# Optimization experiments

Measured on AMD Instinct MI355X. Metric: run time of the kernel, lower is better.

## Reference

```python
import jax, jax.numpy as jnp
import numpy as np
from jax import lax

NUM_ITER = 10
SMOOTH = 1.0


def _minpool(x, wh, ww):
    # stride-1 min pool with SAME padding (pad value +inf, ignored by min)
    return lax.reduce_window(x, np.inf, lax.min, (1, 1, wh, ww), (1, 1, 1, 1), 'SAME')


def _maxpool(x, wh, ww):
    return lax.reduce_window(x, -np.inf, lax.max, (1, 1, wh, ww), (1, 1, 1, 1), 'SAME')


def soft_erode(img):
    # min of separable 3x1 and 1x3 min-pools (== -maxpool(-img) in torch)
    return jnp.minimum(_minpool(img, 3, 1), _minpool(img, 1, 3))


def soft_dilate(img):
    return _maxpool(img, 3, 3)


def soft_open(img):
    return soft_dilate(soft_erode(img))


def soft_skeleton(img, num_iter=NUM_ITER):
    skel = jax.nn.relu(img - soft_open(img))
    x = img
    for _ in range(num_iter):  # fixed small unroll
        x = soft_erode(x)
        delta = jax.nn.relu(x - soft_open(x))
        skel = skel + jax.nn.relu(delta - skel * delta)
    return skel


def setup_inputs() -> dict:
    key = jax.random.key(0)
    k1, k2 = jax.random.split(key)
    pred = jax.random.normal(k1, (32, 1, 512, 512), dtype=jnp.float32)
    target = jax.random.uniform(k2, (32, 1, 512, 512), dtype=jnp.float32)
    return {"pred": pred, "target": target}


def reference(pred, target):
    pred_prob = jax.nn.sigmoid(pred)
    target = target.astype(pred_prob.dtype)
    skel_pred = soft_skeleton(pred_prob, NUM_ITER)
    skel_target = soft_skeleton(target, NUM_ITER)
    tprec = ((skel_pred * target).sum() + SMOOTH) / (skel_pred.sum() + SMOOTH)
    tsens = ((skel_target * pred_prob).sum() + SMOOTH) / (skel_target.sum() + SMOOTH)
    cl_dice = 2 * tprec * tsens / (tprec + tsens + 1e-07)
    return 1.0 - cl_dice
```

## Files before the change

kernel.cpp:

```cpp
#include <hip/hip_runtime.h>

#define H 512
#define W 512
#define TH 64
#define TW 128
#define NT 512
#define SW 168
#define SROWS 90
#define NBANKS 16
#define BANK_STRIDE 16

typedef _Float16 h8 __attribute__((ext_vector_type(8)));
typedef _Float16 h4 __attribute__((ext_vector_type(4)));

__device__ __forceinline__ float sigmf(float x) {
  return __builtin_amdgcn_rcpf(1.0f + __expf(-x));
}
__device__ __forceinline__ float4 ld4(const float* p) { return *(const float4*)p; }

__device__ __forceinline__ h8 max3v(h8 a, h8 b, h8 c) {
  return __builtin_elementwise_max(__builtin_elementwise_max(a, b), c);
}
__device__ __forceinline__ h8 shl1(h8 v, _Float16 e) {
  h8 r = __builtin_shufflevector(v, v, 7, 0, 1, 2, 3, 4, 5, 6);
  r[0] = e;
  return r;
}
__device__ __forceinline__ h8 shr1(h8 v, _Float16 e) {
  h8 r = __builtin_shufflevector(v, v, 1, 2, 3, 4, 5, 6, 7, 0);
  r[7] = e;
  return r;
}
__device__ __forceinline__ _Float16 hi_half(const _Float16* p) {
  unsigned v = *(const unsigned*)p;
  return __builtin_bit_cast(_Float16, (unsigned short)(v >> 16));
}
__device__ __forceinline__ _Float16 lo_half(const _Float16* p) {
  unsigned v = *(const unsigned*)p;
  return __builtin_bit_cast(_Float16, (unsigned short)v);
}
__device__ __forceinline__ _Float16 hmax3(_Float16 a, _Float16 b, _Float16 c) {
  _Float16 m = a > b ? a : b;
  return m > c ? m : c;
}

#define ERODE_AT(r0, gg, oA, oB)                                          \
  {                                                                       \
    const _Float16* s0 = buf + ((r0)-1) * SW + 8 * (GLO + (gg));          \
    h8 a = *(const h8*)(s0);                                              \
    h8 b = *(const h8*)(s0 + SW);                                         \
    h8 c = *(const h8*)(s0 + 2 * SW);                                     \
    h8 d = *(const h8*)(s0 + 3 * SW);                                     \
    _Float16 le0 = hi_half(s0 + SW - 2);                                  \
    _Float16 le1 = hi_half(s0 + 2 * SW - 2);                              \
    _Float16 re0 = lo_half(s0 + SW + 8);                                  \
    _Float16 re1 = lo_half(s0 + 2 * SW + 8);                              \
    h8 m = __builtin_elementwise_min(b, c);                               \
    oA = __builtin_elementwise_min(                                       \
        __builtin_elementwise_min(__builtin_elementwise_min(a, m),        \
                                  shl1(b, le0)),                          \
        shr1(b, re0));                                                    \
    oB = __builtin_elementwise_min(                                       \
        __builtin_elementwise_min(__builtin_elementwise_min(m, d),        \
                                  shl1(c, le1)),                          \
        shr1(c, re1));                                                    \
  }

#define WRITE_AT(r0, gg, oA, oB)                             \
  {                                                          \
    _Float16* d0 = buf + (r0)*SW + 8 * (GLO + (gg));         \
    *(h8*)(d0) = oA;                                         \
    *(h8*)(d0 + SW) = oB;                                    \
  }

template <int G, int GLO>
__device__ __forceinline__ void erode_pass(_Float16* buf, int tid, int rb,
                                           int items) {
  const int rp0 = tid / G;
  const int g0 = tid - rp0 * G;
  const int r00 = rb + 2 * rp0;

  const int it1 = tid + NT;
  const bool a1 = it1 < items;
  const int rp1 = it1 / G;
  const int g1 = it1 - rp1 * G;
  const int r01 = rb + 2 * rp1;

  h8 o00, o01, o10, o11;
  ERODE_AT(r00, g0, o00, o01);
  if (a1) ERODE_AT(r01, g1, o10, o11);

  __syncthreads();

  WRITE_AT(r00, g0, o00, o01);
  if (a1) WRITE_AT(r01, g1, o10, o11);

  __syncthreads();
}

__global__ __launch_bounds__(NT, 4) void cl_skel_kernel(
    const float* __restrict__ pred, const float* __restrict__ target,
    double* __restrict__ sums) {
  __shared__ _Float16 buf[SROWS * SW];
  __shared__ float rbuf[2][NT / 64];

  const int tid = threadIdx.x;
  const int tileIdx = blockIdx.x;
  const int batch = blockIdx.y;
  const bool isPred = (blockIdx.z == 0);
  const int tr = (tileIdx >> 2) * TH;
  const int tc = (tileIdx & 3) * TW;
  const float* __restrict__ img = isPred ? pred : target;
  const float* __restrict__ other = isPred ? target : pred;
  const size_t base = (size_t)batch * (H * W);

  const bool border = (tr == 0) | (tc == 0) | (tr == H - TH) | (tc == W - TW);

  if (!border) {
    for (int it = tid; it < 89 * 40; it += NT) {
      int row = 1 + it / 40, g = it - (row - 1) * 40;
      int gr = tr - 13 + row;
      int gc = tc - 16 + 4 * g;
      float4 v = ld4(&img[base + (size_t)gr * W + gc]);
      if (isPred) {
        v.x = sigmf(v.x); v.y = sigmf(v.y); v.z = sigmf(v.z); v.w = sigmf(v.w);
      }
      h4 hv;
      hv[0] = (_Float16)v.x; hv[1] = (_Float16)v.y;
      hv[2] = (_Float16)v.z; hv[3] = (_Float16)v.w;
      *(h4*)(buf + row * SW + 4 * g) = hv;
    }
  } else {
    for (int it = tid; it < 89 * 40; it += NT) {
      int row = 1 + it / 40, g = it - (row - 1) * 40;
      int gr = min(max(tr - 13 + row, 0), H - 1);
      int gc = tc - 16 + 4 * g;
      float4 v;
      v.x = img[base + (size_t)gr * W + min(max(gc + 0, 0), W - 1)];
      v.y = img[base + (size_t)gr * W + min(max(gc + 1, 0), W - 1)];
      v.z = img[base + (size_t)gr * W + min(max(gc + 2, 0), W - 1)];
      v.w = img[base + (size_t)gr * W + min(max(gc + 3, 0), W - 1)];
      if (isPred) {
        v.x = sigmf(v.x); v.y = sigmf(v.y); v.z = sigmf(v.z); v.w = sigmf(v.w);
      }
      h4 hv;
      hv[0] = (_Float16)v.x; hv[1] = (_Float16)v.y;
      hv[2] = (_Float16)v.z; hv[3] = (_Float16)v.w;
      *(h4*)(buf + row * SW + 4 * g) = hv;
    }
  }
  __syncthreads();

  const int ty = tid >> 3;
  const int tg = tid & 7;
  const int rr = 13 + ty;
  const int c0 = 16 + 16 * tg;

  h8 skelE = (h8)(_Float16)0.0f;
  h8 skelF = (h8)(_Float16)0.0f;

#pragma unroll 1
  for (int R = 11; R >= 1; --R) {
    const int rb = 13 - R;

    const _Float16* ps = buf + rr * SW + c0;
    h8 t0E = *(const h8*)ps;
    h8 t0F = *(const h8*)(ps + 8);

    if (R >= 9) {
      erode_pass<20, 0>(buf, tid, rb, (32 + R) * 20);
    } else {
      erode_pass<18, 1>(buf, tid, rb, (32 + R) * 18);
    }

    {
      const _Float16* pm = buf + (rr - 1) * SW + c0;
      h8 aE = *(const h8*)(pm),          aF = *(const h8*)(pm + 8);
      h8 bE = *(const h8*)(pm + SW),     bF = *(const h8*)(pm + SW + 8);
      h8 cE = *(const h8*)(pm + 2 * SW), cF = *(const h8*)(pm + 2 * SW + 8);
      _Float16 vl = hmax3(hi_half(pm - 2), hi_half(pm + SW - 2),
                          hi_half(pm + 2 * SW - 2));
      _Float16 vr = hmax3(lo_half(pm + 16), lo_half(pm + SW + 16),
                          lo_half(pm + 2 * SW + 16));
      h8 vmE = max3v(aE, bE, cE);
      h8 vmF = max3v(aF, bF, cF);
      h8 hE = max3v(shl1(vmE, vl), vmE, shr1(vmE, vmF[0]));
      h8 hF = max3v(shl1(vmF, vmE[7]), vmF, shr1(vmF, vr));
      h8 z = (h8)(_Float16)0.0f;
      h8 dE = __builtin_elementwise_max(t0E - hE, z);
      h8 dF = __builtin_elementwise_max(t0F - hF, z);
      skelE += __builtin_elementwise_max(dE - skelE * dE, z);
      skelF += __builtin_elementwise_max(dF - skelF * dF, z);
    }
  }

  const float* orow = other + base + (size_t)(tr + ty) * W + tc + 16 * tg;
  float s0 = 0.0f, s1 = 0.0f;
#pragma unroll
  for (int q = 0; q < 4; ++q) {
    float4 o = ld4(orow + 4 * q);
    if (!isPred) {
      o.x = sigmf(o.x); o.y = sigmf(o.y); o.z = sigmf(o.z); o.w = sigmf(o.w);
    }
    float sk0, sk1, sk2, sk3;
    if (q < 2) {
      sk0 = (float)skelE[4 * q + 0]; sk1 = (float)skelE[4 * q + 1];
      sk2 = (float)skelE[4 * q + 2]; sk3 = (float)skelE[4 * q + 3];
    } else {
      sk0 = (float)skelF[4 * q - 8]; sk1 = (float)skelF[4 * q - 7];
      sk2 = (float)skelF[4 * q - 6]; sk3 = (float)skelF[4 * q - 5];
    }
    s0 += (sk0 + sk1) + (sk2 + sk3);
    s1 += (sk0 * o.x + sk1 * o.y) + (sk2 * o.z + sk3 * o.w);
  }

#pragma unroll
  for (int off = 32; off > 0; off >>= 1) {
    s0 += __shfl_down(s0, off, 64);
    s1 += __shfl_down(s1, off, 64);
  }
  const int wave = tid >> 6;
  const int lane = tid & 63;
  if (lane == 0) {
    rbuf[0][wave] = s0;
    rbuf[1][wave] = s1;
  }
  __syncthreads();
  if (tid == 0) {
    float t0 = 0.0f, t1 = 0.0f;
#pragma unroll
    for (int w = 0; w < NT / 64; ++w) {
      t0 += rbuf[0][w];
      t1 += rbuf[1][w];
    }
    const int bank = (int)(blockIdx.x & (NBANKS - 1));
    const int o2 = (isPred ? 0 : 2);
    atomicAdd(&sums[bank * BANK_STRIDE + o2], (double)t0);
    atomicAdd(&sums[bank * BANK_STRIDE + o2 + 1], (double)t1);
  }
}

__global__ void cl_finalize_kernel(const double* __restrict__ sums,
                                   float* __restrict__ out) {
  double s[4] = {0.0, 0.0, 0.0, 0.0};
  for (int b = 0; b < NBANKS; ++b)
    for (int j = 0; j < 4; ++j) s[j] += sums[b * BANK_STRIDE + j];
  double tprec = (s[1] + 1.0) / (s[0] + 1.0);
  double tsens = (s[3] + 1.0) / (s[2] + 1.0);
  double cl = 2.0 * tprec * tsens / (tprec + tsens + 1e-7);
  out[0] = (float)(1.0 - cl);
}

extern "C" void kernel_launch(void* const* d_in, const int* in_sizes, int n_in,
                              void* d_out, int out_size, void* d_ws,
                              size_t ws_size, hipStream_t stream) {
  const float* pred = (const float*)d_in[0];
  const float* target = (const float*)d_in[1];
  double* sums = (double*)d_ws;
  const int batch = in_sizes[0] / (H * W);

  hipMemsetAsync(d_ws, 0, NBANKS * BANK_STRIDE * sizeof(double), stream);
  dim3 grid((H / TH) * (W / TW), batch, 2);
  cl_skel_kernel<<<grid, NT, 0, stream>>>(pred, target, sums);
  cl_finalize_kernel<<<1, 1, 0, stream>>>(sums, (float*)d_out);
}
```

Measured before the change: 197.5 us.

## Double tile height to 128 rows and compute two output rows per thread

Tile height grows from 64 to 128 rows, so the 26-row halo recomputed at each tile edge (loaded and eroded redundantly) makes up a smaller share of each tile's work. Each thread now owns two output rows, and the 3x3 max-pool shares the middle two row maxima between adjacent rows to cut shared-memory loads. The erode pass processes three work items per thread instead of two. Shared memory per block rises to about 51KB, which may reduce occupancy below the 4-blocks launch bound. Fewer blocks also means fewer waves to fill the GPU.

Result: slower. 205.0 us (+3.8%).

```diff
diff --git a/kernel.cpp b/kernel.cpp
--- a/kernel.cpp
+++ b/kernel.cpp
@@ -2,11 +2,11 @@
 
 #define H 512
 #define W 512
-#define TH 64
+#define TH 128
 #define TW 128
 #define NT 512
 #define SW 168
-#define SROWS 90
+#define SROWS 154
 #define NBANKS 16
 #define BANK_STRIDE 16
 
@@ -39,9 +39,8 @@
   unsigned v = *(const unsigned*)p;
   return __builtin_bit_cast(_Float16, (unsigned short)v);
 }
-__device__ __forceinline__ _Float16 hmax3(_Float16 a, _Float16 b, _Float16 c) {
-  _Float16 m = a > b ? a : b;
-  return m > c ? m : c;
+__device__ __forceinline__ _Float16 hmax(_Float16 a, _Float16 b) {
+  return a > b ? a : b;
 }
 
 #define ERODE_AT(r0, gg, oA, oB)                                          \
@@ -81,19 +80,26 @@
   const int r00 = rb + 2 * rp0;
 
   const int it1 = tid + NT;
-  const bool a1 = it1 < items;
   const int rp1 = it1 / G;
   const int g1 = it1 - rp1 * G;
   const int r01 = rb + 2 * rp1;
 
-  h8 o00, o01, o10, o11;
+  const int it2 = tid + 2 * NT;
+  const bool a2 = it2 < items;
+  const int rp2 = it2 / G;
+  const int g2 = it2 - rp2 * G;
+  const int r02 = rb + 2 * rp2;
+
+  h8 o00, o01, o10, o11, o20, o21;
   ERODE_AT(r00, g0, o00, o01);
-  if (a1) ERODE_AT(r01, g1, o10, o11);
+  ERODE_AT(r01, g1, o10, o11);
+  if (a2) ERODE_AT(r02, g2, o20, o21);
 
   __syncthreads();
 
   WRITE_AT(r00, g0, o00, o01);
-  if (a1) WRITE_AT(r01, g1, o10, o11);
+  WRITE_AT(r01, g1, o10, o11);
+  if (a2) WRITE_AT(r02, g2, o20, o21);
 
   __syncthreads();
 }
@@ -117,7 +123,7 @@
   const bool border = (tr == 0) | (tc == 0) | (tr == H - TH) | (tc == W - TW);
 
   if (!border) {
-    for (int it = tid; it < 89 * 40; it += NT) {
+    for (int it = tid; it < 152 * 40; it += NT) {
       int row = 1 + it / 40, g = it - (row - 1) * 40;
       int gr = tr - 13 + row;
       int gc = tc - 16 + 4 * g;
@@ -131,7 +137,7 @@
       *(h4*)(buf + row * SW + 4 * g) = hv;
     }
   } else {
-    for (int it = tid; it < 89 * 40; it += NT) {
+    for (int it = tid; it < 152 * 40; it += NT) {
       int row = 1 + it / 40, g = it - (row - 1) * 40;
       int gr = min(max(tr - 13 + row, 0), H - 1);
       int gc = tc - 16 + 4 * g;
@@ -153,65 +159,107 @@
 
   const int ty = tid >> 3;
   const int tg = tid & 7;
-  const int rr = 13 + ty;
+  const int rr0 = 13 + 2 * ty;
   const int c0 = 16 + 16 * tg;
 
-  h8 skelE = (h8)(_Float16)0.0f;
-  h8 skelF = (h8)(_Float16)0.0f;
+  h8 skelE0 = (h8)(_Float16)0.0f, skelF0 = (h8)(_Float16)0.0f;
+  h8 skelE1 = (h8)(_Float16)0.0f, skelF1 = (h8)(_Float16)0.0f;
 
 #pragma unroll 1
   for (int R = 11; R >= 1; --R) {
     const int rb = 13 - R;
 
-    const _Float16* ps = buf + rr * SW + c0;
-    h8 t0E = *(const h8*)ps;
-    h8 t0F = *(const h8*)(ps + 8);
+    const _Float16* ps = buf + rr0 * SW + c0;
+    h8 t0E0 = *(const h8*)ps,        t0F0 = *(const h8*)(ps + 8);
+    h8 t0E1 = *(const h8*)(ps + SW), t0F1 = *(const h8*)(ps + SW + 8);
 
     if (R >= 9) {
-      erode_pass<20, 0>(buf, tid, rb, (32 + R) * 20);
+      erode_pass<20, 0>(buf, tid, rb, (64 + R) * 20);
     } else {
-      erode_pass<18, 1>(buf, tid, rb, (32 + R) * 18);
+      erode_pass<18, 1>(buf, tid, rb, (64 + R) * 18);
     }
 
     {
-      const _Float16* pm = buf + (rr - 1) * SW + c0;
+      const _Float16* pm = buf + (rr0 - 1) * SW + c0;
       h8 aE = *(const h8*)(pm),          aF = *(const h8*)(pm + 8);
       h8 bE = *(const h8*)(pm + SW),     bF = *(const h8*)(pm + SW + 8);
       h8 cE = *(const h8*)(pm + 2 * SW), cF = *(const h8*)(pm + 2 * SW + 8);
-      _Float16 vl = hmax3(hi_half(pm - 2), hi_half(pm + SW - 2),
-                          hi_half(pm + 2 * SW - 2));
-      _Float16 vr = hmax3(lo_half(pm + 16), lo_half(pm + SW + 16),
-                          lo_half(pm + 2 * SW + 16));
-      h8 vmE = max3v(aE, bE, cE);
-      h8 vmF = max3v(aF, bF, cF);
-      h8 hE = max3v(shl1(vmE, vl), vmE, shr1(vmE, vmF[0]));
-      h8 hF = max3v(shl1(vmF, vmE[7]), vmF, shr1(vmF, vr));
+      h8 dE = *(const h8*)(pm + 3 * SW), dF = *(const h8*)(pm + 3 * SW + 8);
+      _Float16 e0 = hi_half(pm - 2);
+      _Float16 e1 = hi_half(pm + SW - 2);
+      _Float16 e2 = hi_half(pm + 2 * SW - 2);
+      _Float16 e3 = hi_half(pm + 3 * SW - 2);
+      _Float16 w0 = lo_half(pm + 16);
+      _Float16 w1 = lo_half(pm + SW + 16);
+      _Float16 w2 = lo_half(pm + 2 * SW + 16);
+      _Float16 w3 = lo_half(pm + 3 * SW + 16);
+      _Float16 eml = hmax(e1, e2), wml = hmax(w1, w2);
+      _Float16 vl0 = hmax(e0, eml), vl1 = hmax(eml, e3);
+      _Float16 vr0 = hmax(w0, wml), vr1 = hmax(wml, w3);
+      h8 mE = __builtin_elementwise_max(bE, cE);
+      h8 mF = __builtin_elementwise_max(bF, cF);
+      h8 vm0E = __builtin_elementwise_max(aE, mE);
+      h8 vm0F = __builtin_elementwise_max(aF, mF);
+      h8 vm1E = __builtin_elementwise_max(mE, dE);
+      h8 vm1F = __builtin_elementwise_max(mF, dF);
       h8 z = (h8)(_Float16)0.0f;
-      h8 dE = __builtin_elementwise_max(t0E - hE, z);
-      h8 dF = __builtin_elementwise_max(t0F - hF, z);
-      skelE += __builtin_elementwise_max(dE - skelE * dE, z);
-      skelF += __builtin_elementwise_max(dF - skelF * dF, z);
-    }
-  }
-
-  const float* orow = other + base + (size_t)(tr + ty) * W + tc + 16 * tg;
+      {
+        h8 hE = max3v(shl1(vm0E, vl0), vm0E, shr1(vm0E, vm0F[0]));
+        h8 hF = max3v(shl1(vm0F, vm0E[7]), vm0F, shr1(vm0F, vr0));
+        h8 dE_ = __builtin_elementwise_max(t0E0 - hE, z);
+        h8 dF_ = __builtin_elementwise_max(t0F0 - hF, z);
+        skelE0 += __builtin_elementwise_max(dE_ - skelE0 * dE_, z);
+        skelF0 += __builtin_elementwise_max(dF_ - skelF0 * dF_, z);
+      }
+      {
+        h8 hE = max3v(shl1(vm1E, vl1), vm1E, shr1(vm1E, vm1F[0]));
+        h8 hF = max3v(shl1(vm1F, vm1E[7]), vm1F, shr1(vm1F, vr1));
+        h8 dE_ = __builtin_elementwise_max(t0E1 - hE, z);
+        h8 dF_ = __builtin_elementwise_max(t0F1 - hF, z);
+        skelE1 += __builtin_elementwise_max(dE_ - skelE1 * dE_, z);
+        skelF1 += __builtin_elementwise_max(dF_ - skelF1 * dF_, z);
+      }
+    }
+  }
+
   float s0 = 0.0f, s1 = 0.0f;
+  {
+    const float* orow = other + base + (size_t)(tr + 2 * ty) * W + tc + 16 * tg;
 #pragma unroll
-  for (int q = 0; q < 4; ++q) {
-    float4 o = ld4(orow + 4 * q);
-    if (!isPred) {
-      o.x = sigmf(o.x); o.y = sigmf(o.y); o.z = sigmf(o.z); o.w = sigmf(o.w);
-    }
-    float sk0, sk1, sk2, sk3;
-    if (q < 2) {
-      sk0 = (float)skelE[4 * q + 0]; sk1 = (float)skelE[4 * q + 1];
-      sk2 = (float)skelE[4 * q + 2]; sk3 = (float)skelE[4 * q + 3];
-    } else {
-      sk0 = (float)skelF[4 * q - 8]; sk1 = (float)skelF[4 * q - 7];
-      sk2 = (float)skelF[4 * q - 6]; sk3 = (float)skelF[4 * q - 5];
-    }
-    s0 += (sk0 + sk1) + (sk2 + sk3);
-    s1 += (sk0 * o.x + sk1 * o.y) + (sk2 * o.z + sk3 * o.w);
+    for (int q = 0; q < 4; ++q) {
+      float4 o = ld4(orow + 4 * q);
+      if (!isPred) {
+        o.x = sigmf(o.x); o.y = sigmf(o.y); o.z = sigmf(o.z); o.w = sigmf(o.w);
+      }
+      float sk0, sk1, sk2, sk3;
+      if (q < 2) {
+        sk0 = (float)skelE0[4 * q + 0]; sk1 = (float)skelE0[4 * q + 1];
+        sk2 = (float)skelE0[4 * q + 2]; sk3 = (float)skelE0[4 * q + 3];
+      } else {
+        sk0 = (float)skelF0[4 * q - 8]; sk1 = (float)skelF0[4 * q - 7];
+        sk2 = (float)skelF0[4 * q - 6]; sk3 = (float)skelF0[4 * q - 5];
+      }
+      s0 += (sk0 + sk1) + (sk2 + sk3);
+      s1 += (sk0 * o.x + sk1 * o.y) + (sk2 * o.z + sk3 * o.w);
+    }
+    const float* orow1 = orow + W;
+#pragma unroll
+    for (int q = 0; q < 4; ++q) {
+      float4 o = ld4(orow1 + 4 * q);
+      if (!isPred) {
+        o.x = sigmf(o.x); o.y = sigmf(o.y); o.z = sigmf(o.z); o.w = sigmf(o.w);
+      }
+      float sk0, sk1, sk2, sk3;
+      if (q < 2) {
+        sk0 = (float)skelE1[4 * q + 0]; sk1 = (float)skelE1[4 * q + 1];
+        sk2 = (float)skelE1[4 * q + 2]; sk3 = (float)skelE1[4 * q + 3];
+      } else {
+        sk0 = (float)skelF1[4 * q - 8]; sk1 = (float)skelF1[4 * q - 7];
+        sk2 = (float)skelF1[4 * q - 6]; sk3 = (float)skelF1[4 * q - 5];
+      }
+      s0 += (sk0 + sk1) + (sk2 + sk3);
+      s1 += (sk0 * o.x + sk1 * o.y) + (sk2 * o.z + sk3 * o.w);
+    }
   }
 
 #pragma unroll
```
